# Kernel optimization log

Measured on AMD Instinct MI355X. Metric: run time of the kernel, lower is better.

## Reference

```python
import jax, jax.numpy as jnp
import numpy as np

N = 50000
F_IN = 512
H1 = 500
H2 = 100
C = 16
E = 800000


def setup_inputs() -> dict:
    key = jax.random.key(0)
    ks = jax.random.split(key, 8)
    x = jax.random.normal(ks[0], (N, F_IN), dtype=jnp.float32)
    edge_index = jax.random.randint(ks[1], (2, E), 0, N, dtype=jnp.int64)
    W1 = jax.random.normal(ks[2], (F_IN, H1), dtype=jnp.float32) / np.sqrt(F_IN)
    b1 = jnp.zeros((H1,), dtype=jnp.float32)
    W2 = jax.random.normal(ks[3], (H1, H2), dtype=jnp.float32) / np.sqrt(H1)
    b2 = jnp.zeros((H2,), dtype=jnp.float32)
    W3 = jax.random.normal(ks[4], (H2, C), dtype=jnp.float32) / np.sqrt(H2)
    b3 = jnp.zeros((C,), dtype=jnp.float32)
    return {"x": x, "edge_index": edge_index, "W1": W1, "b1": b1,
            "W2": W2, "b2": b2, "W3": W3, "b3": b3}


def _edge_norm(edge_index, num_nodes):
    # add self loops (as in torch add_self_loops), then symmetric degree norm
    loops = jnp.arange(num_nodes, dtype=edge_index.dtype)
    row = jnp.concatenate([edge_index[0], loops])
    col = jnp.concatenate([edge_index[1], loops])
    deg = jax.ops.segment_sum(jnp.ones_like(row, dtype=jnp.float32), row,
                              num_segments=num_nodes)
    dinv = jnp.where(deg > 0, deg ** -0.5, 0.0)  # norm[isinf] = 0
    norm = dinv[row] * dinv[col]
    return row, col, norm


def _graph_conv(x, row, col, norm, W, b, num_nodes):
    h = x @ W + b                                  # [N, out]
    msg = norm[:, None] * h[col]                   # gather + scale, [E', out]
    return jax.ops.segment_sum(msg, row, num_segments=num_nodes)  # SpMM


def reference(x, edge_index, W1, b1, W2, b2, W3, b3):
    num_nodes = x.shape[0]
    row, col, norm = _edge_norm(edge_index, num_nodes)
    h = jnp.tanh(_graph_conv(x, row, col, norm, W1, b1, num_nodes))
    h = jnp.tanh(_graph_conv(h, row, col, norm, W2, b2, num_nodes))
    h = jnp.tanh(_graph_conv(h, row, col, norm, W3, b3, num_nodes))
    return jax.nn.softmax(h, axis=1)
```

## Files before the change

### kernel.cpp

```cpp
#include <hip/hip_runtime.h>
#include <math.h>

#define NN  50000
#define FIN 512
#define HH1 500
#define HH2 100
#define NC  16
#define NE  800000
#define KD  512
#define LDP 40

typedef __attribute__((ext_vector_type(4))) float    f32x4;
typedef __attribute__((ext_vector_type(4))) _Float16 f16x4;
typedef __attribute__((ext_vector_type(8))) _Float16 f16x8;
typedef __attribute__((ext_vector_type(8))) unsigned short u16x8;
typedef __attribute__((ext_vector_type(4))) unsigned short u16x4;


__global__ void zero2_k(int* a, int* b) {
    int i = blockIdx.x * blockDim.x + threadIdx.x;
    if (i < NN) { a[i] = 0; b[i] = 0; }
}

__global__ void hist_k(const int* __restrict__ rows, int* __restrict__ rowcnt) {
    int i = blockIdx.x * blockDim.x + threadIdx.x;
    if (i < NE) atomicAdd(&rowcnt[rows[i]], 1);
}

__global__ void dinv_k(const int* __restrict__ rowcnt, float* __restrict__ dinv) {
    int i = blockIdx.x * blockDim.x + threadIdx.x;
    if (i < NN) dinv[i] = rsqrtf((float)(rowcnt[i] + 1));
}

__global__ __launch_bounds__(1024) void scan1_k(const int* __restrict__ cnt,
                                                int* __restrict__ excl,
                                                int* __restrict__ bsum) {
    __shared__ int s[1024];
    int t = threadIdx.x;
    int i = blockIdx.x * 1024 + t;
    int v = (i < NN) ? cnt[i] : 0;
    s[t] = v;
    __syncthreads();
    #pragma unroll
    for (int off = 1; off < 1024; off <<= 1) {
        int add = (t >= off) ? s[t - off] : 0;
        __syncthreads();
        s[t] += add;
        __syncthreads();
    }
    if (i < NN) excl[i] = s[t] - v;
    if (t == 1023) bsum[blockIdx.x] = s[1023];
}

__global__ void scan2_k(int* bsum, int nb) {
    int lane = threadIdx.x;
    int orig = (lane < nb) ? bsum[lane] : 0;
    int v = orig;
    #pragma unroll
    for (int off = 1; off < 64; off <<= 1) {
        int u = __shfl_up(v, off, 64);
        if (lane >= off) v += u;
    }
    if (lane < nb) bsum[lane] = v - orig;
}

__global__ void scan3_k(const int* __restrict__ excl, const int* __restrict__ bsum,
                        int* __restrict__ ptr) {
    int i = blockIdx.x * 256 + threadIdx.x;
    if (i < NN) ptr[i] = excl[i] + bsum[i >> 10];
}

__global__ void scatter_k(const int* __restrict__ rows, const int* __restrict__ cols,
                          const float* __restrict__ dinv,
                          const int* __restrict__ row_ptr, int* __restrict__ fill,
                          int2* __restrict__ cw) {
    int e = blockIdx.x * blockDim.x + threadIdx.x;
    if (e >= NE) return;
    int r = rows[e], c = cols[e];
    int pos = row_ptr[r] + atomicAdd(&fill[r], 1);
    cw[pos] = make_int2(c, __float_as_int(dinv[r] * dinv[c]));
}


#define R1 (512 * 512)
#define R2 (128 * 512)
#define R3 (128 * 128)

__global__ void wconv3_k(const float* __restrict__ W1, const float* __restrict__ W2,
                         const float* __restrict__ W3, _Float16* __restrict__ Wt1,
                         _Float16* __restrict__ Wt2, _Float16* __restrict__ Wt3)
{
    int idx = blockIdx.x * 256 + threadIdx.x;
    if (idx < R1) {
        int n_ = idx >> 9, kk = idx & 511;
        float v = (n_ < HH1) ? W1[(size_t)kk * HH1 + n_] : 0.0f;
        Wt1[idx] = (_Float16)v;
    } else if (idx < R1 + R2) {
        int j = idx - R1;
        int n_ = j >> 9, kk = j & 511;
        float v = (kk < HH1 && n_ < HH2) ? W2[(size_t)kk * HH2 + n_] : 0.0f;
        Wt2[j] = (_Float16)v;
    } else if (idx < R1 + R2 + R3) {
        int j = idx - R1 - R2;
        int n_ = j >> 7, kk = j & 127;
        float v = (kk < HH2 && n_ < NC) ? W3[(size_t)kk * NC + n_] : 0.0f;
        Wt3[j] = (_Float16)v;
    }
}


template<int AF16, int KDIM, int COUT>
__global__ __launch_bounds__(256) void gemm_f16_k(
    const void* __restrict__ Av, const _Float16* __restrict__ Wt,
    const float* __restrict__ bias, _Float16* __restrict__ Cb,
    int mpad, int n, int m)
{
    __shared__ __align__(16) _Float16 As[128 * LDP];
    __shared__ __align__(16) _Float16 Bs[128 * LDP];

    const float*    Af32 = (const float*)Av;
    const _Float16* Af16 = (const _Float16*)Av;

    int tid  = threadIdx.x;
    int lane = tid & 63;
    int wid  = tid >> 6;
    int wrow = wid & 1, wcol = wid >> 1;
    int lr = lane & 15, q = lane >> 4;
    int row0 = blockIdx.x * 128, col0 = blockIdx.y * 128;

    f32x4 acc[4][4];
    #pragma unroll
    for (int i = 0; i < 4; i++)
        #pragma unroll
        for (int j = 0; j < 4; j++) acc[i][j] = (f32x4){0.f, 0.f, 0.f, 0.f};

    float4 pa32[4];
    u16x8  pa16[2];
    u16x8  pb[2];

    auto load_pf = [&](int kt) {
        if (AF16 == 0) {
            #pragma unroll
            for (int i = 0; i < 4; i++) {
                int idx = tid + i * 256;
                int rr = idx >> 3, c4 = idx & 7;
                int gr = row0 + rr;
                pa32[i] = (gr < n) ? *(const float4*)(Af32 + (size_t)gr * KDIM + kt + c4 * 4)
                                   : make_float4(0.f, 0.f, 0.f, 0.f);
            }
        } else {
            #pragma unroll
            for (int i = 0; i < 2; i++) {
                int idx = tid + i * 256;
                int rr = idx >> 2, c8 = idx & 3;
                int gr = row0 + rr;
                pa16[i] = (gr < n) ? *(const u16x8*)(Af16 + (size_t)gr * KDIM + kt + c8 * 8)
                                   : (u16x8){0, 0, 0, 0, 0, 0, 0, 0};
            }
        }
        #pragma unroll
        for (int i = 0; i < 2; i++) {
            int idx = tid + i * 256;
            int rr = idx >> 2, c8 = idx & 3;
            pb[i] = *(const u16x8*)(Wt + (size_t)(col0 + rr) * KDIM + kt + c8 * 8);
        }
    };

    load_pf(0);

    for (int step = 0; step < KDIM / 32; step++) {
        __syncthreads();
        if (AF16 == 0) {
            #pragma unroll
            for (int i = 0; i < 4; i++) {
                int idx = tid + i * 256;
                int rr = idx >> 3, c4 = idx & 7;
                float4 v = pa32[i];
                f16x4 hv = {(_Float16)v.x, (_Float16)v.y, (_Float16)v.z, (_Float16)v.w};
                *(f16x4*)(As + rr * LDP + c4 * 4) = hv;
            }
        } else {
            #pragma unroll
            for (int i = 0; i < 2; i++) {
                int idx = tid + i * 256;
                int rr = idx >> 2, c8 = idx & 3;
                *(u16x8*)(As + rr * LDP + c8 * 8) = pa16[i];
            }
        }
        #pragma unroll
        for (int i = 0; i < 2; i++) {
            int idx = tid + i * 256;
            int rr = idx >> 2, c8 = idx & 3;
            *(u16x8*)(Bs + rr * LDP + c8 * 8) = pb[i];
        }
        __syncthreads();

        if (step + 1 < KDIM / 32) load_pf((step + 1) * 32);

        f16x8 a[4], b[4];
        #pragma unroll
        for (int t = 0; t < 4; t++) {
            a[t] = *(const f16x8*)(As + (wrow * 64 + t * 16 + lr) * LDP + q * 8);
            b[t] = *(const f16x8*)(Bs + (wcol * 64 + t * 16 + lr) * LDP + q * 8);
        }
        #pragma unroll
        for (int ti = 0; ti < 4; ti++)
            #pragma unroll
            for (int tj = 0; tj < 4; tj++)
                acc[ti][tj] = __builtin_amdgcn_mfma_f32_16x16x32_f16(
                    a[ti], b[tj], acc[ti][tj], 0, 0, 0);
    }

    #pragma unroll
    for (int ti = 0; ti < 4; ti++) {
        #pragma unroll
        for (int tj = 0; tj < 4; tj++) {
            int col = col0 + wcol * 64 + tj * 16 + lr;
            if (col >= mpad) continue;
            bool valid = col < m;
            float bv = valid ? bias[col] : 0.0f;
            #pragma unroll
            for (int p = 0; p < 4; p++) {
                int row = row0 + wrow * 64 + ti * 16 + q * 4 + p;
                if (row < n) {
                    float v = valid ? (acc[ti][tj][p] + bv) : 0.0f;
                    if (COUT == 1) {
                        size_t addr = (size_t)(col >> 8) * ((size_t)NN * 256)
                                    + (size_t)row * 256 + (col & 255);
                        Cb[addr] = (_Float16)v;
                    } else {
                        Cb[(size_t)row * mpad + col] = (_Float16)v;
                    }
                }
            }
        }
    }
}


__device__ __forceinline__ void fma_mix8(float* acc, u16x8 v, float w) {
    union { u16x8 u; unsigned int d[4]; } t; t.u = v;
    #pragma unroll
    for (int k = 0; k < 4; k++) {
        asm("v_fma_mix_f32 %0, %1, %2, %0 op_sel:[0,0,0] op_sel_hi:[1,0,0]"
            : "+v"(acc[2 * k]) : "v"(t.d[k]), "v"(w));
        asm("v_fma_mix_f32 %0, %1, %2, %0 op_sel:[1,0,0] op_sel_hi:[1,0,0]"
            : "+v"(acc[2 * k + 1]) : "v"(t.d[k]), "v"(w));
    }
}

__device__ __forceinline__ void fma_mix4(float* acc, u16x4 v, float w) {
    union { u16x4 u; unsigned int d[2]; } t; t.u = v;
    #pragma unroll
    for (int k = 0; k < 2; k++) {
        asm("v_fma_mix_f32 %0, %1, %2, %0 op_sel:[0,0,0] op_sel_hi:[1,0,0]"
            : "+v"(acc[2 * k]) : "v"(t.d[k]), "v"(w));
        asm("v_fma_mix_f32 %0, %1, %2, %0 op_sel:[1,0,0] op_sel_hi:[1,0,0]"
            : "+v"(acc[2 * k + 1]) : "v"(t.d[k]), "v"(w));
    }
}


__global__ __launch_bounds__(256) void spmm_f16_256_k(
    const int* __restrict__ row_ptr, const int* __restrict__ rowcnt,
    const int2* __restrict__ cw, const float* __restrict__ dinv,
    const _Float16* __restrict__ hc,
    _Float16* __restrict__ outh, int fbase)
{
    int r = blockIdx.x * 4 + (threadIdx.x >> 6);
    int lane = threadIdx.x & 63;
    if (r >= NN) return;

    const u16x4* h4 = (const u16x4*)hc;

    float acc[4];
    #pragma unroll
    for (int i = 0; i < 4; i++) acc[i] = 0.f;

    float d = dinv[r];
    fma_mix4(acc, h4[(size_t)r * 64 + lane], d * d);

    int beg = row_ptr[r], cnt = rowcnt[r];
    for (int base = 0; base < cnt; base += 64) {
        int m = (cnt - base < 64) ? (cnt - base) : 64;
        int2 vc = (lane < m) ? cw[beg + base + lane] : make_int2(0, 0);
        int P = (m + 7) & ~7;
        for (int j = 0; j < P; j += 8) {
            u16x4 vv[8]; float wl[8];
            #pragma unroll
            for (int u = 0; u < 8; u++) {
                int c  = __builtin_amdgcn_readlane(vc.x, j + u);
                int wb = __builtin_amdgcn_readlane(vc.y, j + u);
                wl[u] = __int_as_float(wb);
                vv[u] = h4[(size_t)c * 64 + lane];
            }
            #pragma unroll
            for (int u = 0; u < 8; u++) fma_mix4(acc, vv[u], wl[u]);
        }
    }

    int f0 = fbase + lane * 4;
    f16x4 o;
    #pragma unroll
    for (int i = 0; i < 4; i++)
        o[i] = (_Float16)((f0 + i < HH1) ? tanhf(acc[i]) : 0.0f);
    __builtin_nontemporal_store(o, (f16x4*)(outh + (size_t)r * KD + f0));
}


__global__ __launch_bounds__(256) void spmm_f16_100_k(
    const int* __restrict__ row_ptr, const int* __restrict__ rowcnt,
    const int2* __restrict__ cw, const float* __restrict__ dinv,
    const _Float16* __restrict__ hb, _Float16* __restrict__ outh)
{
    int r = blockIdx.x * 16 + (threadIdx.x >> 4);
    int lane = threadIdx.x & 15;
    if (r >= NN) return;

    const u16x8* h8 = (const u16x8*)hb;

    float acc[8];
    #pragma unroll
    for (int i = 0; i < 8; i++) acc[i] = 0.f;

    float d = dinv[r];
    fma_mix8(acc, h8[(size_t)r * 16 + lane], d * d);

    int beg = row_ptr[r], cnt = rowcnt[r];
    int j = 0;
    for (; j + 7 < cnt; j += 8) {
        int2  e[8];
        u16x8 v[8];
        #pragma unroll
        for (int u = 0; u < 8; u++) e[u] = cw[beg + j + u];
        #pragma unroll
        for (int u = 0; u < 8; u++) v[u] = h8[(size_t)e[u].x * 16 + lane];
        #pragma unroll
        for (int u = 0; u < 8; u++) fma_mix8(acc, v[u], __int_as_float(e[u].y));
    }
    for (; j < cnt; j++) {
        int2 e = cw[beg + j];
        fma_mix8(acc, h8[(size_t)e.x * 16 + lane], __int_as_float(e.y));
    }

    int f0 = lane * 8;
    f16x8 o;
    #pragma unroll
    for (int i = 0; i < 8; i++)
        o[i] = (_Float16)((f0 + i < HH2) ? tanhf(acc[i]) : 0.0f);
    __builtin_nontemporal_store(o, (f16x8*)(outh + (size_t)r * 128 + f0));
}


__global__ __launch_bounds__(256) void spmm3h_k(
    const int* __restrict__ row_ptr, const int* __restrict__ rowcnt,
    const int2* __restrict__ cw, const float* __restrict__ dinv,
    const _Float16* __restrict__ hb, float* __restrict__ out)
{
    int r = blockIdx.x * 128 + (threadIdx.x >> 1);
    int lane = threadIdx.x & 1;
    if (r >= NN) return;

    const u16x8* h8 = (const u16x8*)hb;

    float acc[8];
    #pragma unroll
    for (int i = 0; i < 8; i++) acc[i] = 0.f;

    float d = dinv[r];
    fma_mix8(acc, h8[(size_t)r * 2 + lane], d * d);

    int beg = row_ptr[r], cnt = rowcnt[r];
    int j = 0;
    for (; j + 3 < cnt; j += 4) {
        int2  e0 = cw[beg + j],     e1 = cw[beg + j + 1];
        int2  e2 = cw[beg + j + 2], e3 = cw[beg + j + 3];
        u16x8 v0 = h8[(size_t)e0.x * 2 + lane];
        u16x8 v1 = h8[(size_t)e1.x * 2 + lane];
        u16x8 v2 = h8[(size_t)e2.x * 2 + lane];
        u16x8 v3 = h8[(size_t)e3.x * 2 + lane];
        fma_mix8(acc, v0, __int_as_float(e0.y));
        fma_mix8(acc, v1, __int_as_float(e1.y));
        fma_mix8(acc, v2, __int_as_float(e2.y));
        fma_mix8(acc, v3, __int_as_float(e3.y));
    }
    for (; j < cnt; j++) {
        int2 e = cw[beg + j];
        fma_mix8(acc, h8[(size_t)e.x * 2 + lane], __int_as_float(e.y));
    }

    float* o = out + (size_t)r * NC + lane * 8;
    f32x4 a0 = {acc[0], acc[1], acc[2], acc[3]};
    f32x4 a1 = {acc[4], acc[5], acc[6], acc[7]};
    __builtin_nontemporal_store(a0, (f32x4*)o);
    __builtin_nontemporal_store(a1, (f32x4*)(o + 4));
}

__global__ void tanh_softmax_k(const float* __restrict__ in, float* __restrict__ out) {
    int r = blockIdx.x * blockDim.x + threadIdx.x;
    if (r >= NN) return;
    float v[NC];
    float mx = -1e30f;
    #pragma unroll
    for (int j = 0; j < NC; j++) {
        v[j] = tanhf(in[r * NC + j]);
        mx = fmaxf(mx, v[j]);
    }
    float s = 0.0f;
    #pragma unroll
    for (int j = 0; j < NC; j++) { v[j] = expf(v[j] - mx); s += v[j]; }
    float inv = 1.0f / s;
    #pragma unroll
    for (int j = 0; j < NC; j++) out[r * NC + j] = v[j] * inv;
}


extern "C" void kernel_launch(void* const* d_in, const int* in_sizes, int n_in,
                              void* d_out, int out_size, void* d_ws, size_t ws_size,
                              hipStream_t stream)
{
    const float* x  = (const float*)d_in[0];
    const int*   ei = (const int*)d_in[1];
    const float* W1 = (const float*)d_in[2];
    const float* b1 = (const float*)d_in[3];
    const float* W2 = (const float*)d_in[4];
    const float* b2 = (const float*)d_in[5];
    const float* W3 = (const float*)d_in[6];
    const float* b3 = (const float*)d_in[7];
    float* out = (float*)d_out;

    const int* rows = ei;
    const int* cols = ei + NE;

    char* p = (char*)d_ws;
    float*     dinv    = (float*)p;     p += (size_t)NN * 4;
    int*       rowcnt  = (int*)p;       p += (size_t)NN * 4;
    int*       row_ptr = (int*)p;       p += (size_t)NN * 4;
    int*       fill    = (int*)p;       p += (size_t)NN * 4;
    int*       excl    = (int*)p;       p += (size_t)NN * 4;
    int*       bsum    = (int*)p;       p += (size_t)256 * 4;
    int2*      cw      = (int2*)p;      p += (size_t)NE * 8;
    float*     B3      = (float*)p;     p += (size_t)NN * NC * 4;
    _Float16*  A1h     = (_Float16*)p;  p += (size_t)NN * KD * 2;
    _Float16*  h1h     = (_Float16*)p;  p += (size_t)NN * KD * 2;
    _Float16*  A2h     = (_Float16*)p;  p += (size_t)NN * 128 * 2;
    _Float16*  h2h     = (_Float16*)p;  p += (size_t)NN * 128 * 2;
    _Float16*  A3h     = (_Float16*)p;  p += (size_t)NN * NC * 2;
    _Float16*  Wt1     = (_Float16*)p;  p += (size_t)R1 * 2;
    _Float16*  Wt2     = (_Float16*)p;  p += (size_t)R2 * 2;
    _Float16*  Wt3     = (_Float16*)p;  p += (size_t)R3 * 2;

    const int T = 256;
    const int NB = (NN + 1023) / 1024;

    wconv3_k<<<(R1 + R2 + R3) / 256, T, 0, stream>>>(W1, W2, W3, Wt1, Wt2, Wt3);
    zero2_k<<<(NN + T - 1) / T, T, 0, stream>>>(rowcnt, fill);
    hist_k<<<(NE + T - 1) / T, T, 0, stream>>>(rows, rowcnt);
    dinv_k<<<(NN + T - 1) / T, T, 0, stream>>>(rowcnt, dinv);
    scan1_k<<<NB, 1024, 0, stream>>>(rowcnt, excl, bsum);
    scan2_k<<<1, 64, 0, stream>>>(bsum, NB);
    scan3_k<<<(NN + T - 1) / T, T, 0, stream>>>(excl, bsum, row_ptr);
    scatter_k<<<(NE + T - 1) / T, T, 0, stream>>>(rows, cols, dinv, row_ptr, fill, cw);

    {
        dim3 g((NN + 127) / 128, 4);
        gemm_f16_k<0, 512, 1><<<g, T, 0, stream>>>(x, Wt1, b1, A1h, KD, NN, HH1);
        spmm_f16_256_k<<<(NN + 3) / 4, T, 0, stream>>>(row_ptr, rowcnt, cw, dinv,
                                                       A1h, h1h, 0);
        spmm_f16_256_k<<<(NN + 3) / 4, T, 0, stream>>>(row_ptr, rowcnt, cw, dinv,
                                                       A1h + (size_t)NN * 256, h1h, 256);
    }
    {
        dim3 g((NN + 127) / 128, 1);
        gemm_f16_k<1, 512, 0><<<g, T, 0, stream>>>(h1h, Wt2, b2, A2h, 128, NN, HH2);
        spmm_f16_100_k<<<(NN + 15) / 16, T, 0, stream>>>(row_ptr, rowcnt, cw,
                                                         dinv, A2h, h2h);
    }
    {
        dim3 g((NN + 127) / 128, 1);
        gemm_f16_k<1, 128, 0><<<g, T, 0, stream>>>(h2h, Wt3, b3, A3h, NC, NN, NC);
        spmm3h_k<<<(NN + 127) / 128, T, 0, stream>>>(row_ptr, rowcnt, cw,
                                                     dinv, A3h, B3);
        tanh_softmax_k<<<(NN + T - 1) / T, T, 0, stream>>>(B3, out);
    }
}
```

Baseline: 551.0 us.

## Add full-width layer-1 GEMM kernel so each x tile is read once

```diff
diff --git a/kernel.cpp b/kernel.cpp
--- a/kernel.cpp
+++ b/kernel.cpp
@@ -109,7 +109,105 @@
 }
 
 
-template<int AF16, int KDIM, int COUT>
+__global__ __launch_bounds__(256, 2) void gemm1_wide_k(
+    const float* __restrict__ A, const _Float16* __restrict__ Wt,
+    const float* __restrict__ bias, _Float16* __restrict__ Cb, int n)
+{
+    __shared__ __align__(16) _Float16 As[64 * LDP];
+    __shared__ __align__(16) _Float16 Bs[512 * LDP];
+
+    int tid  = threadIdx.x;
+    int lane = tid & 63;
+    int w    = tid >> 6;
+    int lr = lane & 15, q = lane >> 4;
+    int row0 = blockIdx.x * 64;
+
+    f32x4 acc[4][8];
+    #pragma unroll
+    for (int i = 0; i < 4; i++)
+        #pragma unroll
+        for (int j = 0; j < 8; j++) acc[i][j] = (f32x4){0.f, 0.f, 0.f, 0.f};
+
+    float4 pa[2];
+    u16x8  pb[8];
+
+    auto load_pf = [&](int kt) {
+        #pragma unroll
+        for (int i = 0; i < 2; i++) {
+            int idx = tid + i * 256;
+            int rr = idx >> 3, c4 = idx & 7;
+            int gr = row0 + rr;
+            pa[i] = (gr < n) ? *(const float4*)(A + (size_t)gr * 512 + kt + c4 * 4)
+                             : make_float4(0.f, 0.f, 0.f, 0.f);
+        }
+        #pragma unroll
+        for (int i = 0; i < 8; i++) {
+            int idx = tid + i * 256;
+            int rr = idx >> 2, c8 = idx & 3;
+            pb[i] = *(const u16x8*)(Wt + (size_t)rr * 512 + kt + c8 * 8);
+        }
+    };
+
+    load_pf(0);
+
+    for (int step = 0; step < 16; step++) {
+        __syncthreads();
+        #pragma unroll
+        for (int i = 0; i < 2; i++) {
+            int idx = tid + i * 256;
+            int rr = idx >> 3, c4 = idx & 7;
+            float4 v = pa[i];
+            f16x4 hv = {(_Float16)v.x, (_Float16)v.y, (_Float16)v.z, (_Float16)v.w};
+            *(f16x4*)(As + rr * LDP + c4 * 4) = hv;
+        }
+        #pragma unroll
+        for (int i = 0; i < 8; i++) {
+            int idx = tid + i * 256;
+            int rr = idx >> 2, c8 = idx & 3;
+            *(u16x8*)(Bs + rr * LDP + c8 * 8) = pb[i];
+        }
+        __syncthreads();
+
+        if (step + 1 < 16) load_pf((step + 1) * 32);
+
+        f16x8 a[4], b[8];
+        #pragma unroll
+        for (int t = 0; t < 4; t++)
+            a[t] = *(const f16x8*)(As + (t * 16 + lr) * LDP + q * 8);
+        #pragma unroll
+        for (int t = 0; t < 8; t++)
+            b[t] = *(const f16x8*)(Bs + (w * 128 + t * 16 + lr) * LDP + q * 8);
+
+        #pragma unroll
+        for (int ti = 0; ti < 4; ti++)
+            #pragma unroll
+            for (int tj = 0; tj < 8; tj++)
+                acc[ti][tj] = __builtin_amdgcn_mfma_f32_16x16x32_f16(
+                    a[ti], b[tj], acc[ti][tj], 0, 0, 0);
+    }
+
+    #pragma unroll
+    for (int ti = 0; ti < 4; ti++) {
+        #pragma unroll
+        for (int tj = 0; tj < 8; tj++) {
+            int col = w * 128 + tj * 16 + lr;
+            bool valid = col < HH1;
+            float bv = valid ? bias[col] : 0.0f;
+            size_t cbase = (size_t)(col >> 8) * ((size_t)NN * 256) + (col & 255);
+            #pragma unroll
+            for (int p = 0; p < 4; p++) {
+                int row = row0 + ti * 16 + q * 4 + p;
+                if (row < n) {
+                    float v = valid ? (acc[ti][tj][p] + bv) : 0.0f;
+                    Cb[cbase + (size_t)row * 256] = (_Float16)v;
+                }
+            }
+        }
+    }
+}
+
+
+template<int AF16, int KDIM>
 __global__ __launch_bounds__(256) void gemm_f16_k(
     const void* __restrict__ Av, const _Float16* __restrict__ Wt,
     const float* __restrict__ bias, _Float16* __restrict__ Cb,
@@ -224,13 +322,7 @@
                 int row = row0 + wrow * 64 + ti * 16 + q * 4 + p;
                 if (row < n) {
                     float v = valid ? (acc[ti][tj][p] + bv) : 0.0f;
-                    if (COUT == 1) {
-                        size_t addr = (size_t)(col >> 8) * ((size_t)NN * 256)
-                                    + (size_t)row * 256 + (col & 255);
-                        Cb[addr] = (_Float16)v;
-                    } else {
-                        Cb[(size_t)row * mpad + col] = (_Float16)v;
-                    }
+                    Cb[(size_t)row * mpad + col] = (_Float16)v;
                 }
             }
         }
@@ -463,8 +555,7 @@
     scatter_k<<<(NE + T - 1) / T, T, 0, stream>>>(rows, cols, dinv, row_ptr, fill, cw);
 
     {
-        dim3 g((NN + 127) / 128, 4);
-        gemm_f16_k<0, 512, 1><<<g, T, 0, stream>>>(x, Wt1, b1, A1h, KD, NN, HH1);
+        gemm1_wide_k<<<(NN + 63) / 64, T, 0, stream>>>(x, Wt1, b1, A1h, NN);
         spmm_f16_256_k<<<(NN + 3) / 4, T, 0, stream>>>(row_ptr, rowcnt, cw, dinv,
                                                        A1h, h1h, 0);
         spmm_f16_256_k<<<(NN + 3) / 4, T, 0, stream>>>(row_ptr, rowcnt, cw, dinv,
@@ -472,13 +563,13 @@
     }
     {
         dim3 g((NN + 127) / 128, 1);
-        gemm_f16_k<1, 512, 0><<<g, T, 0, stream>>>(h1h, Wt2, b2, A2h, 128, NN, HH2);
+        gemm_f16_k<1, 512><<<g, T, 0, stream>>>(h1h, Wt2, b2, A2h, 128, NN, HH2);
         spmm_f16_100_k<<<(NN + 15) / 16, T, 0, stream>>>(row_ptr, rowcnt, cw,
                                                          dinv, A2h, h2h);
     }
     {
         dim3 g((NN + 127) / 128, 1);
-        gemm_f16_k<1, 128, 0><<<g, T, 0, stream>>>(h2h, Wt3, b3, A3h, NC, NN, NC);
+        gemm_f16_k<1, 128><<<g, T, 0, stream>>>(h2h, Wt3, b3, A3h, NC, NN, NC);
         spmm3h_k<<<(NN + 127) / 128, T, 0, stream>>>(row_ptr, rowcnt, cw,
                                                      dinv, A3h, B3);
         tanh_softmax_k<<<(NN + T - 1) / T, T, 0, stream>>>(B3, out);
```

New measurement: 547.9 us. No clear change (-0.6%).

## Rewrite GEMMs with direct global-to-LDS loads, swizzle, double buffering, pre-converted x

Applied to the files above, without the earlier changes.

```diff
diff --git a/kernel.cpp b/kernel.cpp
--- a/kernel.cpp
+++ b/kernel.cpp
@@ -8,7 +8,6 @@
 #define NC  16
 #define NE  800000
 #define KD  512
-#define LDP 40
 
 typedef __attribute__((ext_vector_type(4))) float    f32x4;
 typedef __attribute__((ext_vector_type(4))) _Float16 f16x4;
@@ -109,119 +108,105 @@
 }
 
 
-template<int AF16, int KDIM, int COUT>
-__global__ __launch_bounds__(256) void gemm_f16_k(
-    const void* __restrict__ Av, const _Float16* __restrict__ Wt,
+__global__ __launch_bounds__(256) void cvtx_k(const float4* __restrict__ x,
+                                              f16x8* __restrict__ xh) {
+    int i = blockIdx.x * 256 + threadIdx.x;
+    float4 v0 = x[2 * i], v1 = x[2 * i + 1];
+    f16x8 h = {(_Float16)v0.x, (_Float16)v0.y, (_Float16)v0.z, (_Float16)v0.w,
+               (_Float16)v1.x, (_Float16)v1.y, (_Float16)v1.z, (_Float16)v1.w};
+    __builtin_nontemporal_store(h, xh + i);
+}
+
+
+typedef unsigned int u32g;
+
+__device__ __forceinline__ void g2l16(const void* g, void* l) {
+    __builtin_amdgcn_global_load_lds(
+        (const __attribute__((address_space(1))) u32g*)g,
+        (__attribute__((address_space(3))) u32g*)l, 16, 0, 0);
+}
+
+template<int BCOLS, int COUT, int KK>
+__global__ __launch_bounds__(256, 3) void gemm_lds_k(
+    const _Float16* __restrict__ A,
+    const _Float16* __restrict__ Wt,
     const float* __restrict__ bias, _Float16* __restrict__ Cb,
     int mpad, int n, int m)
 {
-    __shared__ __align__(16) _Float16 As[128 * LDP];
-    __shared__ __align__(16) _Float16 Bs[128 * LDP];
-
-    const float*    Af32 = (const float*)Av;
-    const _Float16* Af16 = (const _Float16*)Av;
+    constexpr int NBF   = BCOLS / 64;
+    constexpr int WC    = BCOLS / 4;
+    constexpr int NSTEP = KK / 32;
+
+    __shared__ __align__(16) _Float16 As[2][64 * 32];
+    __shared__ __align__(16) _Float16 Bs[2][BCOLS * 32];
 
     int tid  = threadIdx.x;
     int lane = tid & 63;
-    int wid  = tid >> 6;
-    int wrow = wid & 1, wcol = wid >> 1;
+    int w    = tid >> 6;
     int lr = lane & 15, q = lane >> 4;
-    int row0 = blockIdx.x * 128, col0 = blockIdx.y * 128;
-
-    f32x4 acc[4][4];
+    int row0 = blockIdx.x * 64;
+    int col0 = blockIdx.y * BCOLS;
+
+    f32x4 acc[4][NBF];
     #pragma unroll
     for (int i = 0; i < 4; i++)
         #pragma unroll
-        for (int j = 0; j < 4; j++) acc[i][j] = (f32x4){0.f, 0.f, 0.f, 0.f};
-
-    float4 pa32[4];
-    u16x8  pa16[2];
-    u16x8  pb[2];
-
-    auto load_pf = [&](int kt) {
-        if (AF16 == 0) {
-            #pragma unroll
-            for (int i = 0; i < 4; i++) {
-                int idx = tid + i * 256;
-                int rr = idx >> 3, c4 = idx & 7;
-                int gr = row0 + rr;
-                pa32[i] = (gr < n) ? *(const float4*)(Af32 + (size_t)gr * KDIM + kt + c4 * 4)
-                                   : make_float4(0.f, 0.f, 0.f, 0.f);
-            }
-        } else {
-            #pragma unroll
-            for (int i = 0; i < 2; i++) {
-                int idx = tid + i * 256;
-                int rr = idx >> 2, c8 = idx & 3;
-                int gr = row0 + rr;
-                pa16[i] = (gr < n) ? *(const u16x8*)(Af16 + (size_t)gr * KDIM + kt + c8 * 8)
-                                   : (u16x8){0, 0, 0, 0, 0, 0, 0, 0};
-            }
-        }
-        #pragma unroll
-        for (int i = 0; i < 2; i++) {
-            int idx = tid + i * 256;
+        for (int j = 0; j < NBF; j++) acc[i][j] = (f32x4){0.f, 0.f, 0.f, 0.f};
+
+    auto stage = [&](int kt, int bf) {
+        {
+            int rr = tid >> 2, c8 = tid & 3;
+            int c8s = c8 ^ ((rr >> 1) & 3);
+            int gr = row0 + rr; if (gr >= n) gr = n - 1;
+            g2l16(A + (size_t)gr * KK + kt + c8s * 8, &As[bf][tid * 8]);
+        }
+        #pragma unroll
+        for (int i = 0; i < NBF; i++) {
+            int idx = i * 256 + tid;
             int rr = idx >> 2, c8 = idx & 3;
-            pb[i] = *(const u16x8*)(Wt + (size_t)(col0 + rr) * KDIM + kt + c8 * 8);
+            int c8s = c8 ^ ((rr >> 1) & 3);
+            g2l16(Wt + (size_t)(col0 + rr) * KK + kt + c8s * 8, &Bs[bf][idx * 8]);
         }
     };
 
-    load_pf(0);
-
-    for (int step = 0; step < KDIM / 32; step++) {
+    stage(0, 0);
+    int bf = 0;
+    #pragma unroll
+    for (int step = 0; step < NSTEP; step++) {
         __syncthreads();
-        if (AF16 == 0) {
-            #pragma unroll
-            for (int i = 0; i < 4; i++) {
-                int idx = tid + i * 256;
-                int rr = idx >> 3, c4 = idx & 7;
-                float4 v = pa32[i];
-                f16x4 hv = {(_Float16)v.x, (_Float16)v.y, (_Float16)v.z, (_Float16)v.w};
-                *(f16x4*)(As + rr * LDP + c4 * 4) = hv;
-            }
-        } else {
-            #pragma unroll
-            for (int i = 0; i < 2; i++) {
-                int idx = tid + i * 256;
-                int rr = idx >> 2, c8 = idx & 3;
-                *(u16x8*)(As + rr * LDP + c8 * 8) = pa16[i];
-            }
-        }
-        #pragma unroll
-        for (int i = 0; i < 2; i++) {
-            int idx = tid + i * 256;
-            int rr = idx >> 2, c8 = idx & 3;
-            *(u16x8*)(Bs + rr * LDP + c8 * 8) = pb[i];
-        }
-        __syncthreads();
-
-        if (step + 1 < KDIM / 32) load_pf((step + 1) * 32);
-
-        f16x8 a[4], b[4];
+        if (step + 1 < NSTEP) stage((step + 1) * 32, bf ^ 1);
+
+        f16x8 a[4], b[NBF];
         #pragma unroll
         for (int t = 0; t < 4; t++) {
-            a[t] = *(const f16x8*)(As + (wrow * 64 + t * 16 + lr) * LDP + q * 8);
-            b[t] = *(const f16x8*)(Bs + (wcol * 64 + t * 16 + lr) * LDP + q * 8);
+            int row = t * 16 + lr;
+            a[t] = *(const f16x8*)&As[bf][(row * 4 + (q ^ ((row >> 1) & 3))) * 8];
+        }
+        #pragma unroll
+        for (int t = 0; t < NBF; t++) {
+            int row = w * WC + t * 16 + lr;
+            b[t] = *(const f16x8*)&Bs[bf][(row * 4 + (q ^ ((row >> 1) & 3))) * 8];
         }
         #pragma unroll
         for (int ti = 0; ti < 4; ti++)
             #pragma unroll
-            for (int tj = 0; tj < 4; tj++)
+            for (int tj = 0; tj < NBF; tj++)
                 acc[ti][tj] = __builtin_amdgcn_mfma_f32_16x16x32_f16(
                     a[ti], b[tj], acc[ti][tj], 0, 0, 0);
+        bf ^= 1;
     }
 
     #pragma unroll
     for (int ti = 0; ti < 4; ti++) {
         #pragma unroll
-        for (int tj = 0; tj < 4; tj++) {
-            int col = col0 + wcol * 64 + tj * 16 + lr;
-            if (col >= mpad) continue;
+        for (int tj = 0; tj < NBF; tj++) {
+            int col = col0 + w * WC + tj * 16 + lr;
+            if (COUT == 0 && col >= mpad) continue;
             bool valid = col < m;
             float bv = valid ? bias[col] : 0.0f;
             #pragma unroll
             for (int p = 0; p < 4; p++) {
-                int row = row0 + wrow * 64 + ti * 16 + q * 4 + p;
+                int row = row0 + ti * 16 + q * 4 + p;
                 if (row < n) {
                     float v = valid ? (acc[ti][tj][p] + bv) : 0.0f;
                     if (COUT == 1) {
@@ -450,10 +435,14 @@
     _Float16*  Wt2     = (_Float16*)p;  p += (size_t)R2 * 2;
     _Float16*  Wt3     = (_Float16*)p;  p += (size_t)R3 * 2;
 
+    _Float16* xh = h1h;
+
     const int T = 256;
     const int NB = (NN + 1023) / 1024;
+    const int GB = (NN + 63) / 64;
 
     wconv3_k<<<(R1 + R2 + R3) / 256, T, 0, stream>>>(W1, W2, W3, Wt1, Wt2, Wt3);
+    cvtx_k<<<(NN * FIN / 8) / 256, T, 0, stream>>>((const float4*)x, (f16x8*)xh);
     zero2_k<<<(NN + T - 1) / T, T, 0, stream>>>(rowcnt, fill);
     hist_k<<<(NE + T - 1) / T, T, 0, stream>>>(rows, rowcnt);
     dinv_k<<<(NN + T - 1) / T, T, 0, stream>>>(rowcnt, dinv);
@@ -463,22 +452,22 @@
     scatter_k<<<(NE + T - 1) / T, T, 0, stream>>>(rows, cols, dinv, row_ptr, fill, cw);
 
     {
-        dim3 g((NN + 127) / 128, 4);
-        gemm_f16_k<0, 512, 1><<<g, T, 0, stream>>>(x, Wt1, b1, A1h, KD, NN, HH1);
+        gemm_lds_k<256, 1, 512><<<dim3(GB, 2), T, 0, stream>>>(
+            xh, Wt1, b1, A1h, KD, NN, HH1);
         spmm_f16_256_k<<<(NN + 3) / 4, T, 0, stream>>>(row_ptr, rowcnt, cw, dinv,
                                                        A1h, h1h, 0);
         spmm_f16_256_k<<<(NN + 3) / 4, T, 0, stream>>>(row_ptr, rowcnt, cw, dinv,
                                                        A1h + (size_t)NN * 256, h1h, 256);
     }
     {
-        dim3 g((NN + 127) / 128, 1);
-        gemm_f16_k<1, 512, 0><<<g, T, 0, stream>>>(h1h, Wt2, b2, A2h, 128, NN, HH2);
+        gemm_lds_k<128, 0, 512><<<dim3(GB, 1), T, 0, stream>>>(
+            h1h, Wt2, b2, A2h, 128, NN, HH2);
         spmm_f16_100_k<<<(NN + 15) / 16, T, 0, stream>>>(row_ptr, rowcnt, cw,
                                                          dinv, A2h, h2h);
     }
     {
-        dim3 g((NN + 127) / 128, 1);
-        gemm_f16_k<1, 128, 0><<<g, T, 0, stream>>>(h2h, Wt3, b3, A3h, NC, NN, NC);
+        gemm_lds_k<64, 0, 128><<<dim3(GB, 1), T, 0, stream>>>(
+            h2h, Wt3, b3, A3h, NC, NN, NC);
         spmm3h_k<<<(NN + 127) / 128, T, 0, stream>>>(row_ptr, rowcnt, cw,
                                                      dinv, A3h, B3);
         tanh_softmax_k<<<(NN + T - 1) / T, T, 0, stream>>>(B3, out);
```

Result: no change. 546.6 us (-0.8%).
